# Kernel optimization log

Measured on AMD Instinct MI355X. Metric: run time of the kernel, lower is better.

The kernel has to match this reference:

```python
import jax, jax.numpy as jnp
import numpy as np
import math

NSAMPLE = 16
ATTN_TEMP = 1.0
LEAKY = 0.1
BN_EPS = 1e-5


def _knn(k, query, ref):
    # query [B,Nq,3], ref [B,Nr,3] -> idx [B,Nq,k] (indices into ref, nearest first)
    d = (jnp.sum(query * query, -1)[:, :, None]
         + jnp.sum(ref * ref, -1)[:, None, :]
         - 2.0 * jnp.einsum('bqc,brc->bqr', query, ref))
    _, idx = jax.lax.top_k(-d, k)
    return idx


def _gather(pts, idx):
    # pts [B,N,C], idx [B,M,K] -> [B,M,K,C]
    return jax.vmap(lambda p, i: p[i])(pts, idx)


def _bn_eval(x, g, b):
    # eval-mode BatchNorm2d with running_mean=0, running_var=1
    return x * (g / jnp.sqrt(1.0 + BN_EPS)) + b


def _leaky(x):
    return jnp.where(x >= 0, x, LEAKY * x)


def setup_inputs() -> dict:
    key = jax.random.key(0)
    ks = jax.random.split(key, 25)
    B, N, D, Cm, H = 2, 4096, 64, 64, 8
    f = jax.random.normal
    inp = {
        'xyz1': f(ks[0], (B, 3, N), jnp.float32),
        'xyz2': f(ks[1], (B, 3, N), jnp.float32),
        'xyz2w': f(ks[2], (B, 3, N), jnp.float32),
        'points1': f(ks[3], (B, D, N), jnp.float32),
        'points2': f(ks[4], (B, D, N), jnp.float32),
        'mlp_W0': f(ks[5], (Cm, 2 * D + 3), jnp.float32) * 0.1,
        'mlp_b0': f(ks[6], (Cm,), jnp.float32) * 0.05,
        'mlp_W1': f(ks[7], (Cm, Cm), jnp.float32) * 0.1,
        'mlp_b1': f(ks[8], (Cm,), jnp.float32) * 0.05,
        'wn_W0': f(ks[9], (H, 3), jnp.float32) * 0.3,
        'wn_b0': f(ks[10], (H,), jnp.float32) * 0.05,
        'wn_g0': jax.random.uniform(ks[11], (H,), jnp.float32, 0.5, 1.5),
        'wn_be0': f(ks[12], (H,), jnp.float32) * 0.05,
        'wn_W1': f(ks[13], (H, H), jnp.float32) * 0.3,
        'wn_b1': f(ks[14], (H,), jnp.float32) * 0.05,
        'wn_g1': jax.random.uniform(ks[15], (H,), jnp.float32, 0.5, 1.5),
        'wn_be1': f(ks[16], (H,), jnp.float32) * 0.05,
        'wn_W2': f(ks[17], (Cm, H), jnp.float32) * 0.3,
        'wn_b2': f(ks[18], (Cm,), jnp.float32) * 0.05,
        'wn_g2': jax.random.uniform(ks[19], (Cm,), jnp.float32, 0.5, 1.5),
        'wn_be2': f(ks[20], (Cm,), jnp.float32) * 0.05,
    }
    return inp


def reference(xyz1, xyz2, xyz2w, points1, points2,
              mlp_W0, mlp_b0, mlp_W1, mlp_b1,
              wn_W0, wn_b0, wn_g0, wn_be0,
              wn_W1, wn_b1, wn_g1, wn_be1,
              wn_W2, wn_b2, wn_g2, wn_be2):
    K = NSAMPLE
    B, C, N1 = xyz1.shape  # C == 3
    p1 = xyz1.transpose(0, 2, 1)    # [B,N1,3]
    p2 = xyz2.transpose(0, 2, 1)
    p2w = xyz2w.transpose(0, 2, 1)
    f1 = points1.transpose(0, 2, 1)  # [B,N1,D]
    f2 = points2.transpose(0, 2, 1)

    def mlp(f):
        f = _leaky(jnp.einsum('bnkc,oc->bnko', f, mlp_W0) + mlp_b0)
        f = _leaky(jnp.einsum('bnkc,oc->bnko', f, mlp_W1) + mlp_b1)
        return f

    idx = _knn(K, p1, p2)
    dir_xyz = _gather(p2, idx) - p1[:, :, None, :]          # [B,N1,K,3]
    idxw = _knn(K, p1, p2w)
    dir_xyzw = _gather(p2w, idxw) - p1[:, :, None, :]

    g1 = jnp.broadcast_to(f1[:, :, None, :], (B, N1, K, f1.shape[-1]))
    feat = mlp(jnp.concatenate([g1, _gather(f2, idx), dir_xyz], -1))    # [B,N1,K,Cm]
    featw = mlp(jnp.concatenate([g1, _gather(f2, idxw), dir_xyzw], -1))  # [B,N1,K,Cm]

    # per-channel K x K attention, contracted over all N1 points
    wqk = jnp.einsum('bnkc,bnlc->bckl', feat, featw)        # [B,Cm,K,K]
    wqk = jnp.clip(jax.nn.softmax(wqk / ATTN_TEMP, -1) / math.sqrt(C), 1e-10)
    # sum over trailing K is pushed into the attention matrix (same math)
    costw = jnp.einsum('bnlc,bcl->bcn', featw, wqk.sum(-1))  # [B,Cm,N1]
    cost = jnp.einsum('bnlc,bcl->bcn', feat, wqk.sum(-2))    # [B,Cm,N1]

    # self-neighborhood aggregation with WeightNet (bn=True, eval mode)
    idx_s = _knn(K, p1, p1)
    dir_s = _gather(p1, idx_s) - p1[:, :, None, :]           # [B,N1,K,3]
    h = jax.nn.relu(_bn_eval(jnp.einsum('bnkc,oc->bnko', dir_s, wn_W0) + wn_b0, wn_g0, wn_be0))
    h = jax.nn.relu(_bn_eval(jnp.einsum('bnkc,oc->bnko', h, wn_W1) + wn_b1, wn_g1, wn_be1))
    w = jax.nn.relu(_bn_eval(jnp.einsum('bnkc,oc->bnko', h, wn_W2) + wn_b2, wn_g2, wn_be2))  # [B,N1,K,Cm]

    grouped = _gather(cost.transpose(0, 2, 1), idx_s) + _gather(costw.transpose(0, 2, 1), idx_s)  # [B,N1,K,Cm]
    return jnp.einsum('bnkc,bnkc->bcn', w, grouped)          # [B,Cm,N1]
```

## Files before the change

### kernel.cpp

```cpp
#include <hip/hip_runtime.h>
#include <math.h>

#define B_  2
#define N_  4096
#define K_  16
#define D_  64
#define CM_ 64
#define H_  8

#define NSEG  8
#define SEGSZ (N_ / NSEG)
#define QPB   256
#define LIM   16
#define BATCH 8
#define TAUS  512

__device__ __forceinline__ void ce64(unsigned long long& a, unsigned long long& b) {
    bool sw = b < a;
    unsigned long long lo = sw ? b : a;
    unsigned long long hi = sw ? a : b;
    a = lo; b = hi;
}
__device__ __forceinline__ void cef(float& a, float& b) {
    float lo = fminf(a, b), hi = fmaxf(a, b);
    a = lo; b = hi;
}

#define SORT16_(e, CE) do { \
    CE(e[0],e[1]); CE(e[2],e[3]); CE(e[4],e[5]); CE(e[6],e[7]); \
    CE(e[8],e[9]); CE(e[10],e[11]); CE(e[12],e[13]); CE(e[14],e[15]); \
    CE(e[0],e[2]); CE(e[1],e[3]); CE(e[4],e[6]); CE(e[5],e[7]); \
    CE(e[8],e[10]); CE(e[9],e[11]); CE(e[12],e[14]); CE(e[13],e[15]); \
    CE(e[1],e[2]); CE(e[5],e[6]); CE(e[9],e[10]); CE(e[13],e[14]); \
    CE(e[0],e[4]); CE(e[1],e[5]); CE(e[2],e[6]); CE(e[3],e[7]); \
    CE(e[8],e[12]); CE(e[9],e[13]); CE(e[10],e[14]); CE(e[11],e[15]); \
    CE(e[2],e[4]); CE(e[3],e[5]); CE(e[10],e[12]); CE(e[11],e[13]); \
    CE(e[1],e[2]); CE(e[3],e[4]); CE(e[5],e[6]); \
    CE(e[9],e[10]); CE(e[11],e[12]); CE(e[13],e[14]); \
    CE(e[0],e[8]); CE(e[1],e[9]); CE(e[2],e[10]); CE(e[3],e[11]); \
    CE(e[4],e[12]); CE(e[5],e[13]); CE(e[6],e[14]); CE(e[7],e[15]); \
    CE(e[4],e[8]); CE(e[5],e[9]); CE(e[6],e[10]); CE(e[7],e[11]); \
    CE(e[2],e[4]); CE(e[3],e[5]); CE(e[6],e[8]); CE(e[7],e[9]); \
    CE(e[10],e[12]); CE(e[11],e[13]); \
    CE(e[1],e[2]); CE(e[3],e[4]); CE(e[5],e[6]); CE(e[7],e[8]); \
    CE(e[9],e[10]); CE(e[11],e[12]); CE(e[13],e[14]); \
} while (0)

#define BMERGE16_(d, CE) do { \
    CE(d[0],d[8]); CE(d[1],d[9]); CE(d[2],d[10]); CE(d[3],d[11]); \
    CE(d[4],d[12]); CE(d[5],d[13]); CE(d[6],d[14]); CE(d[7],d[15]); \
    CE(d[0],d[4]); CE(d[1],d[5]); CE(d[2],d[6]); CE(d[3],d[7]); \
    CE(d[8],d[12]); CE(d[9],d[13]); CE(d[10],d[14]); CE(d[11],d[15]); \
    CE(d[0],d[2]); CE(d[1],d[3]); CE(d[4],d[6]); CE(d[5],d[7]); \
    CE(d[8],d[10]); CE(d[9],d[11]); CE(d[12],d[14]); CE(d[13],d[15]); \
    CE(d[0],d[1]); CE(d[2],d[3]); CE(d[4],d[5]); CE(d[6],d[7]); \
    CE(d[8],d[9]); CE(d[10],d[11]); CE(d[12],d[13]); CE(d[14],d[15]); \
} while (0)

__global__ __launch_bounds__(256) void knn_tau_kernel(
    const float* __restrict__ xyz1, const float* __restrict__ xyz2,
    const float* __restrict__ xyz2w,
    float* __restrict__ tauBuf)
{
    const int b = blockIdx.y, which = blockIdx.z;
    const float* q = xyz1 + (size_t)b * 3 * N_;
    const float* r = (which == 0 ? xyz2 : (which == 1 ? xyz2w : xyz1)) + (size_t)b * 3 * N_;

    const int tid = threadIdx.x;
    const int qi = blockIdx.x * QPB + tid;
    const float qx = q[qi], qy = q[N_ + qi], qz = q[2 * N_ + qi];
    const float qq = qx * qx + qy * qy + qz * qz;

    __shared__ float4 tile[TAUS];
    __shared__ float  bufS[LIM * QPB];

    float bd[K_];
#pragma unroll
    for (int i = 0; i < K_; ++i) bd[i] = 3.4e38f;
    float tau = 3.4e38f;
    float c = 0.5f * (qq - tau);
    c -= fabsf(c) * 0.0009765625f + 1e-20f;
    int cnt = 0;

    for (int j = tid; j < TAUS; j += QPB) {
        float x = r[j], y = r[N_ + j], z = r[2 * N_ + j];
        tile[j] = make_float4(x, y, z, -0.5f * (x * x + y * y + z * z));
    }
    __syncthreads();

    auto compactF = [&](int m_end) {
        float e[16];
#pragma unroll
        for (int m = 0; m < 16; ++m) {
            float sv = bufS[m * QPB + tid];
            float dv = fmaxf(qq - 2.0f * sv, 0.0f);
            e[m] = (m < m_end) ? dv : 3.4e38f;
        }
        SORT16_(e, cef);
#pragma unroll
        for (int i = 0; i < 16; ++i) bd[i] = fminf(bd[i], e[15 - i]);
        BMERGE16_(bd, cef);
        tau = fminf(tau, bd[K_ - 1]);
        c = 0.5f * (qq - tau);
        c -= fabsf(c) * 0.0009765625f + 1e-20f;
    };

    for (int j0 = 0; j0 < TAUS; j0 += BATCH) {
        float s8[BATCH];
#pragma unroll
        for (int u = 0; u < BATCH; ++u) {
            float4 t = tile[j0 + u];
            s8[u] = qx * t.x + (qy * t.y + (qz * t.z + t.w));
        }
#pragma unroll
        for (int u = 0; u < BATCH; ++u) {
            bufS[cnt * QPB + tid] = s8[u];
            cnt += (s8[u] > c) ? 1 : 0;
        }
        if (__any(cnt > 8)) { compactF(cnt); cnt = 0; }
    }
    if (__any(cnt != 0)) compactF(cnt);

    tauBuf[((size_t)b * 3 + which) * N_ + qi] = bd[K_ - 1];
}

__global__ __launch_bounds__(256) void knn_seg_kernel(
    const float* __restrict__ xyz1, const float* __restrict__ xyz2,
    const float* __restrict__ xyz2w,
    const float* __restrict__ tauBuf,
    float* __restrict__ segD, int* __restrict__ segI)
{
    const int b = blockIdx.y;
    const int which = blockIdx.z >> 3;
    const int seg   = blockIdx.z & 7;
    const float* q = xyz1 + (size_t)b * 3 * N_;
    const float* r = (which == 0 ? xyz2 : (which == 1 ? xyz2w : xyz1)) + (size_t)b * 3 * N_;

    const int tid = threadIdx.x;
    const int qi = blockIdx.x * QPB + tid;
    const float qx = q[qi], qy = q[N_ + qi], qz = q[2 * N_ + qi];
    const float qq = qx * qx + qy * qy + qz * qz;

    __shared__ float4 tile[SEGSZ];
    __shared__ int    bufI[LIM * QPB];

    unsigned long long bd[K_];
#pragma unroll
    for (int i = 0; i < K_; ++i) bd[i] = ~0ull;
    float tau = tauBuf[((size_t)b * 3 + which) * N_ + qi];
    float c = 0.5f * (qq - tau);
    c -= fabsf(c) * 0.0009765625f + 1e-20f;
    int cnt = 0;

    const int base0 = seg * SEGSZ;
    for (int j = tid; j < SEGSZ; j += QPB) {
        float x = r[base0 + j], y = r[N_ + base0 + j], z = r[2 * N_ + base0 + j];
        tile[j] = make_float4(x, y, z, -0.5f * (x * x + y * y + z * z));
    }
    __syncthreads();

    auto compact = [&](int m_end) {
        unsigned long long e[16];
#pragma unroll
        for (int m = 0; m < 16; ++m) {
            int j = bufI[m * QPB + tid] & (SEGSZ - 1);
            float4 t = tile[j];
            float dot = qx * t.x + qy * t.y + qz * t.z;
            float rr = -2.0f * t.w;
            float dv = fmaxf((qq + rr) - 2.0f * dot, 0.0f);
            unsigned long long key =
                ((unsigned long long)__float_as_uint(dv) << 32)
                | (unsigned)(base0 + j);
            e[m] = (m < m_end) ? key : ~0ull;
        }
        SORT16_(e, ce64);
#pragma unroll
        for (int i = 0; i < 16; ++i) {
            unsigned long long cand = e[15 - i];
            if (cand < bd[i]) bd[i] = cand;
        }
        BMERGE16_(bd, ce64);
        tau = fminf(tau, __uint_as_float((unsigned)(bd[K_ - 1] >> 32)));
        c = 0.5f * (qq - tau);
        c -= fabsf(c) * 0.0009765625f + 1e-20f;
    };

    for (int j0 = 0; j0 < SEGSZ; j0 += BATCH) {
        float s8[BATCH];
#pragma unroll
        for (int u = 0; u < BATCH; ++u) {
            float4 t = tile[j0 + u];
            s8[u] = qx * t.x + (qy * t.y + (qz * t.z + t.w));
        }
#pragma unroll
        for (int u = 0; u < BATCH; ++u) {
            bufI[cnt * QPB + tid] = j0 + u;
            cnt += (s8[u] > c) ? 1 : 0;
        }
        if (__any(cnt > 8)) { compact(cnt); cnt = 0; }
    }
    if (__any(cnt != 0)) compact(cnt);

    const size_t ob = (((size_t)(b * 3 + which) * NSEG + seg) * K_) * N_ + qi;
#pragma unroll
    for (int i = 0; i < K_; ++i) {
        segD[ob + (size_t)i * N_] = __uint_as_float((unsigned)(bd[i] >> 32));
        segI[ob + (size_t)i * N_] = (int)(unsigned)bd[i];
    }
}

__global__ __launch_bounds__(256) void knn_merge_kernel(
    const float* __restrict__ segD, const int* __restrict__ segI,
    int* __restrict__ idxA, int* __restrict__ idxB, int* __restrict__ idxS)
{
    const int b = blockIdx.y, which = blockIdx.z;
    const int qi = blockIdx.x * 256 + threadIdx.x;
    unsigned long long m[K_];
#pragma unroll
    for (int i = 0; i < K_; ++i) m[i] = ~0ull;
    for (int s = 0; s < NSEG; ++s) {
        const size_t ob = (((size_t)(b * 3 + which) * NSEG + s) * K_) * N_ + qi;
        for (int e = 0; e < K_; ++e) {
            unsigned long long key =
                ((unsigned long long)__float_as_uint(segD[ob + (size_t)e * N_]) << 32)
                | (unsigned)segI[ob + (size_t)e * N_];
            if (key >= m[K_ - 1]) break;
            m[K_ - 1] = key;
#pragma unroll
            for (int i = K_ - 1; i > 0; --i) {
                if (m[i] < m[i - 1]) {
                    unsigned long long t = m[i]; m[i] = m[i - 1]; m[i - 1] = t;
                }
            }
        }
    }
    int* outp = (which == 0 ? idxA : (which == 1 ? idxB : idxS));
    int* op = outp + ((size_t)b * N_ + qi) * K_;
#pragma unroll
    for (int i = 0; i < K_; ++i) op[i] = (int)(unsigned)m[i];
}

__global__ __launch_bounds__(256) void pre_gemm_kernel(
    const float* __restrict__ points1, const float* __restrict__ points2,
    const float* __restrict__ W0,
    float* __restrict__ G1, float* __restrict__ P2)
{
    const int b = blockIdx.y, which = blockIdx.z;
    const float* src = which ? points2 : points1;
    float* dst = which ? P2 : G1;
    const int woff = which ? 64 : 0;
    const int n0 = blockIdx.x * 64;
    const int tid = threadIdx.x;

    __shared__ float sW[64 * 65];
    __shared__ float sA[64 * 68];

    for (int i = tid; i < 4096; i += 256) {
        int c = i & 63, o = i >> 6;
        sW[c * 65 + o] = W0[o * 131 + woff + c];
    }
    for (int i = tid; i < 4096; i += 256) {
        int n = i & 63, c = i >> 6;
        sA[c * 68 + n] = src[((size_t)b * 64 + c) * N_ + n0 + n];
    }
    __syncthreads();

    const int o = tid & 63, qg = tid >> 6;
    float acc[16];
#pragma unroll
    for (int j = 0; j < 16; ++j) acc[j] = 0.f;
    for (int c = 0; c < 64; ++c) {
        float w = sW[c * 65 + o];
        const float4* ap = (const float4*)&sA[c * 68 + qg * 16];
#pragma unroll
        for (int m = 0; m < 4; ++m) {
            float4 a4 = ap[m];
            acc[4 * m + 0] += w * a4.x;
            acc[4 * m + 1] += w * a4.y;
            acc[4 * m + 2] += w * a4.z;
            acc[4 * m + 3] += w * a4.w;
        }
    }
#pragma unroll
    for (int j = 0; j < 16; ++j)
        dst[((size_t)b * N_ + n0 + qg * 16 + j) * 64 + o] = acc[j];
}

__global__ __launch_bounds__(256) void mlp2_kernel(
    const float* __restrict__ xyz1, const float* __restrict__ xyz2,
    const float* __restrict__ xyz2w,
    const int* __restrict__ idxA, const int* __restrict__ idxB,
    const float* __restrict__ G1, const float* __restrict__ P2,
    const float* __restrict__ W0, const float* __restrict__ b0,
    const float* __restrict__ W1, const float* __restrict__ b1,
    float* __restrict__ feat, float* __restrict__ featw)
{
    const int b = blockIdx.y, which = blockIdx.z;
    const int* idx = which ? idxB : idxA;
    const float* refxyz = (which ? xyz2w : xyz2) + (size_t)b * 3 * N_;
    float* outp = which ? featw : feat;
    const int n0 = blockIdx.x * 8;
    const int tid = threadIdx.x;
    const int w = tid >> 6, lane = tid & 63;

    __shared__ float sh0[64 * 132];
    __shared__ float sW1[64 * 68];
    __shared__ float sWc[3 * 64];
    __shared__ float sB0[64];
    __shared__ float sQ[3][8];
    __shared__ int   sIdx[128];

    for (int i = tid; i < 4096; i += 256) {
        int c = i & 63, o = i >> 6;
        sW1[c * 68 + o] = W1[o * 64 + c];
    }
    if (tid < 192) { int m = tid >> 6, o = tid & 63; sWc[m * 64 + o] = W0[o * 131 + 128 + m]; }
    if (tid < 64) sB0[tid] = b0[tid];
    if (tid < 24) { int m = tid >> 3, j = tid & 7; sQ[m][j] = xyz1[((size_t)b * 3 + m) * N_ + n0 + j]; }
    if (tid < 128) sIdx[tid] = idx[((size_t)b * N_ + n0 + (tid >> 4)) * K_ + (tid & 15)];
    __syncthreads();

    {
        const int o = lane;
        const float wc0 = sWc[o], wc1 = sWc[64 + o], wc2 = sWc[128 + o];
        const float bb0 = sB0[o];
#pragma unroll
        for (int p = 0; p < 2; ++p) {
            const int pl = w * 2 + p;
            const float g1 = G1[((size_t)b * N_ + n0 + pl) * 64 + o];
            const float qx = sQ[0][pl], qy = sQ[1][pl], qz = sQ[2][pl];
            for (int k = 0; k < K_; ++k) {
                const int row = pl * K_ + k;
                const int ii = sIdx[row];
                float p2 = P2[((size_t)b * N_ + ii) * 64 + o];
                float dx = refxyz[ii] - qx;
                float dy = refxyz[N_ + ii] - qy;
                float dz = refxyz[2 * N_ + ii] - qz;
                float h = g1 + p2 + dx * wc0 + dy * wc1 + dz * wc2 + bb0;
                h = h >= 0.f ? h : 0.1f * h;
                sh0[o * 132 + row] = h;
            }
        }
    }
    __syncthreads();

    const int lr = lane >> 3, lo = lane & 7;
    float accv[4][8];
    {
        float4 bva = *(const float4*)&b1[lo * 8];
        float4 bvb = *(const float4*)&b1[lo * 8 + 4];
#pragma unroll
        for (int dr = 0; dr < 4; ++dr) {
            accv[dr][0] = bva.x; accv[dr][1] = bva.y; accv[dr][2] = bva.z; accv[dr][3] = bva.w;
            accv[dr][4] = bvb.x; accv[dr][5] = bvb.y; accv[dr][6] = bvb.z; accv[dr][7] = bvb.w;
        }
    }
    for (int c = 0; c < 64; ++c) {
        float4 a4 = *(const float4*)&sh0[c * 132 + w * 32 + lr * 4];
        float4 wa = *(const float4*)&sW1[c * 68 + lo * 8];
        float4 wb = *(const float4*)&sW1[c * 68 + lo * 8 + 4];
        float av[4] = {a4.x, a4.y, a4.z, a4.w};
        float wv[8] = {wa.x, wa.y, wa.z, wa.w, wb.x, wb.y, wb.z, wb.w};
#pragma unroll
        for (int dr = 0; dr < 4; ++dr)
#pragma unroll
            for (int j = 0; j < 8; ++j)
                accv[dr][j] += av[dr] * wv[j];
    }
#pragma unroll
    for (int dr = 0; dr < 4; ++dr) {
        const int row = w * 32 + lr * 4 + dr;
        const int pl = row >> 4, k = row & 15;
        float o8[8];
#pragma unroll
        for (int j = 0; j < 8; ++j) {
            float v = accv[dr][j];
            o8[j] = v >= 0.f ? v : 0.1f * v;
        }
        float* op = outp + (((size_t)b * N_ + n0 + pl) * K_ + k) * 64 + lo * 8;
        *(float4*)op = make_float4(o8[0], o8[1], o8[2], o8[3]);
        *(float4*)(op + 4) = make_float4(o8[4], o8[5], o8[6], o8[7]);
    }
}

#define NCHUNK 32
#define CG 16
#define NITER ((N_ / NCHUNK) / 16)

__global__ __launch_bounds__(256) void attn_partial_kernel(
    const float* __restrict__ feat, const float* __restrict__ featw,
    float* __restrict__ partial)
{
    const int chunk = blockIdx.x;
    const int b = blockIdx.y >> 2;
    const int c0 = (blockIdx.y & 3) * CG;
    const int tid = threadIdx.x;
    const int k = tid >> 4, c = tid & 15;

    __shared__ float sf[16 * 16 * 17];
    __shared__ float sfw[16 * 16 * 20];

    float acc[K_];
#pragma unroll
    for (int l = 0; l < K_; ++l) acc[l] = 0.f;

    const int n0 = chunk * (N_ / NCHUNK);
    float rf[16], rfw[16];

    auto LOADG = [&](int ns) {
#pragma unroll
        for (int t = 0; t < 16; ++t) {
            int i = tid + t * 256;
            int nn = i >> 8, p = (i >> 4) & 15, qv = i & 15;
            size_t base = (((size_t)b * N_ + n0 + ns + nn) * K_ + p) * CM_ + c0 + qv;
            rf[t]  = feat[base];
            rfw[t] = featw[base];
        }
    };
    auto STORE = [&]() {
#pragma unroll
        for (int t = 0; t < 16; ++t) {
            int i = tid + t * 256;
            int nn = i >> 8, p = (i >> 4) & 15, qv = i & 15;
            sf[nn * 272 + p * 17 + qv]  = rf[t];
            sfw[nn * 320 + qv * 20 + p] = rfw[t];
        }
    };

    LOADG(0);
    for (int it = 0; it < NITER; ++it) {
        __syncthreads();
        STORE();
        __syncthreads();
        if (it + 1 < NITER) LOADG((it + 1) * 16);
#pragma unroll
        for (int nn = 0; nn < 16; ++nn) {
            float f = sf[nn * 272 + k * 17 + c];
            const float4* fp = (const float4*)&sfw[nn * 320 + c * 20];
#pragma unroll
            for (int m = 0; m < 4; ++m) {
                float4 v = fp[m];
                acc[4 * m + 0] += f * v.x;
                acc[4 * m + 1] += f * v.y;
                acc[4 * m + 2] += f * v.z;
                acc[4 * m + 3] += f * v.w;
            }
        }
    }
    float* pp = partial + ((((size_t)b * NCHUNK + chunk) * CM_ + (c0 + c)) * K_ + k) * K_;
#pragma unroll
    for (int m = 0; m < 4; ++m)
        *(float4*)(pp + 4 * m) = make_float4(acc[4 * m], acc[4 * m + 1], acc[4 * m + 2], acc[4 * m + 3]);
}

__global__ __launch_bounds__(256) void attn_reduce_kernel(
    const float* __restrict__ partial,
    float* __restrict__ rowsum, float* __restrict__ colsum)
{
    const int c = blockIdx.x, b = blockIdx.y;
    const int tid = threadIdx.x;
    const int k = tid >> 4, l = tid & 15;
    __shared__ float smat[K_][K_ + 1];

    float acc = 0.f;
#pragma unroll
    for (int ch = 0; ch < NCHUNK; ++ch)
        acc += partial[((((size_t)b * NCHUNK + ch) * CM_ + c) * K_ + k) * K_ + l];

    float m = acc;
#pragma unroll
    for (int off = 8; off >= 1; off >>= 1) m = fmaxf(m, __shfl_xor(m, off, 16));
    float e = expf(acc - m);
    float s = e;
#pragma unroll
    for (int off = 8; off >= 1; off >>= 1) s += __shfl_xor(s, off, 16);
    float sm = fmaxf((e / s) * 0.57735026918962576f, 1e-10f);

    float rs = sm;
#pragma unroll
    for (int off = 8; off >= 1; off >>= 1) rs += __shfl_xor(rs, off, 16);
    if (l == 0) rowsum[((size_t)b * CM_ + c) * K_ + k] = rs;

    smat[k][l] = sm;
    __syncthreads();
    if (tid < K_) {
        float cs = 0.f;
#pragma unroll
        for (int kk = 0; kk < K_; ++kk) cs += smat[kk][tid];
        colsum[((size_t)b * CM_ + c) * K_ + tid] = cs;
    }
}

__global__ __launch_bounds__(256) void cost_kernel(
    const float* __restrict__ feat, const float* __restrict__ featw,
    const float* __restrict__ rowsum, const float* __restrict__ colsum,
    float* __restrict__ costT, float* __restrict__ costwT)
{
    const int b = blockIdx.y;
    const int tid = threadIdx.x;
    __shared__ float scs[64][K_ + 1], srs[64][K_ + 1];
    for (int i = tid; i < 64 * K_; i += 256) {
        int cc = i >> 4, j = i & 15;
        scs[cc][j] = colsum[((size_t)b * CM_ + cc) * K_ + j];
        srs[cc][j] = rowsum[((size_t)b * CM_ + cc) * K_ + j];
    }
    __syncthreads();
    const int ng = tid >> 6, c = tid & 63;
    const int n = blockIdx.x * 4 + ng;
    const float* fp  = feat  + (((size_t)b * N_ + n) * K_) * 64 + c;
    const float* fwp = featw + (((size_t)b * N_ + n) * K_) * 64 + c;
    float a = 0.f, aw = 0.f;
#pragma unroll
    for (int j = 0; j < K_; ++j) {
        a  += fp[j * 64]  * scs[c][j];
        aw += fwp[j * 64] * srs[c][j];
    }
    costT[((size_t)b * N_ + n) * 64 + c]  = a;
    costwT[((size_t)b * N_ + n) * 64 + c] = aw;
}

__global__ __launch_bounds__(256) void final_kernel(
    const float* __restrict__ xyz1,
    const int* __restrict__ idxS,
    const float* __restrict__ costT, const float* __restrict__ costwT,
    const float* __restrict__ wn_W0, const float* __restrict__ wn_b0,
    const float* __restrict__ wn_g0, const float* __restrict__ wn_be0,
    const float* __restrict__ wn_W1, const float* __restrict__ wn_b1,
    const float* __restrict__ wn_g1, const float* __restrict__ wn_be1,
    const float* __restrict__ wn_W2, const float* __restrict__ wn_b2,
    const float* __restrict__ wn_g2, const float* __restrict__ wn_be2,
    float* __restrict__ out)
{
    const int b = blockIdx.y;
    const int tid = threadIdx.x;
    const int ng = tid >> 6, c = tid & 63;
    const int n = blockIdx.x * 4 + ng;
    const float invs = 1.0f / sqrtf(1.0f + 1e-5f);

    __shared__ int   sI[4][K_];
    __shared__ float sH1[4][K_][H_];

    if (c < K_) {
        const int k = c;
        const float* qb = xyz1 + (size_t)b * 3 * N_;
        int ii = idxS[((size_t)b * N_ + n) * K_ + k];
        sI[ng][k] = ii;
        float dx = qb[ii] - qb[n];
        float dy = qb[N_ + ii] - qb[N_ + n];
        float dz = qb[2 * N_ + ii] - qb[2 * N_ + n];
        float h0[H_];
#pragma unroll
        for (int o = 0; o < H_; ++o) {
            float v = wn_W0[o * 3] * dx + wn_W0[o * 3 + 1] * dy + wn_W0[o * 3 + 2] * dz + wn_b0[o];
            v = v * (wn_g0[o] * invs) + wn_be0[o];
            h0[o] = fmaxf(v, 0.f);
        }
#pragma unroll
        for (int o = 0; o < H_; ++o) {
            float v = wn_b1[o];
#pragma unroll
            for (int j = 0; j < H_; ++j) v += wn_W1[o * H_ + j] * h0[j];
            v = v * (wn_g1[o] * invs) + wn_be1[o];
            sH1[ng][k][o] = fmaxf(v, 0.f);
        }
    }
    __syncthreads();

    float w2r[H_];
#pragma unroll
    for (int j = 0; j < H_; ++j) w2r[j] = wn_W2[c * H_ + j];
    const float b2v = wn_b2[c];
    const float s2v = wn_g2[c] * invs;
    const float t2v = wn_be2[c];

    float acc = 0.f;
#pragma unroll
    for (int k = 0; k < K_; ++k) {
        float v = b2v;
#pragma unroll
        for (int j = 0; j < H_; ++j) v += w2r[j] * sH1[ng][k][j];
        float wv = fmaxf(v * s2v + t2v, 0.f);
        int ii = sI[ng][k];
        size_t base = ((size_t)b * N_ + ii) * 64 + c;
        acc += wv * (costT[base] + costwT[base]);
    }
    out[((size_t)b * CM_ + c) * N_ + n] = acc;
}

extern "C" void kernel_launch(void* const* d_in, const int* in_sizes, int n_in,
                              void* d_out, int out_size, void* d_ws, size_t ws_size,
                              hipStream_t stream)
{
    const float* xyz1    = (const float*)d_in[0];
    const float* xyz2    = (const float*)d_in[1];
    const float* xyz2w   = (const float*)d_in[2];
    const float* points1 = (const float*)d_in[3];
    const float* points2 = (const float*)d_in[4];
    const float* mlp_W0  = (const float*)d_in[5];
    const float* mlp_b0  = (const float*)d_in[6];
    const float* mlp_W1  = (const float*)d_in[7];
    const float* mlp_b1  = (const float*)d_in[8];
    const float* wn_W0   = (const float*)d_in[9];
    const float* wn_b0   = (const float*)d_in[10];
    const float* wn_g0   = (const float*)d_in[11];
    const float* wn_be0  = (const float*)d_in[12];
    const float* wn_W1   = (const float*)d_in[13];
    const float* wn_b1   = (const float*)d_in[14];
    const float* wn_g1   = (const float*)d_in[15];
    const float* wn_be1  = (const float*)d_in[16];
    const float* wn_W2   = (const float*)d_in[17];
    const float* wn_b2   = (const float*)d_in[18];
    const float* wn_g2   = (const float*)d_in[19];
    const float* wn_be2  = (const float*)d_in[20];
    float* out = (float*)d_out;

    char* ws = (char*)d_ws;
    size_t off = 0;
    auto alloc = [&](size_t bytes) -> void* {
        void* p = ws + off;
        off += (bytes + 255) & ~(size_t)255;
        return p;
    };
    int*   idxA   = (int*)  alloc((size_t)B_ * N_ * K_ * sizeof(int));
    int*   idxB   = (int*)  alloc((size_t)B_ * N_ * K_ * sizeof(int));
    int*   idxS   = (int*)  alloc((size_t)B_ * N_ * K_ * sizeof(int));
    float* tauBuf = (float*)alloc((size_t)B_ * 3 * N_ * sizeof(float));
    float* feat   = (float*)alloc((size_t)B_ * N_ * K_ * CM_ * sizeof(float));
    float* featw  = (float*)alloc((size_t)B_ * N_ * K_ * CM_ * sizeof(float));
    float* rowsum = (float*)alloc((size_t)B_ * CM_ * K_ * sizeof(float));
    float* colsum = (float*)alloc((size_t)B_ * CM_ * K_ * sizeof(float));
    float* costT  = (float*)alloc((size_t)B_ * N_ * CM_ * sizeof(float));
    float* costwT = (float*)alloc((size_t)B_ * N_ * CM_ * sizeof(float));
    (void)ws_size; (void)in_sizes; (void)n_in; (void)out_size;

    float* segD    = feat;
    int*   segI    = (int*)featw;
    float* G1      = costT;
    float* P2      = costwT;
    float* partial = costT;

    pre_gemm_kernel<<<dim3(N_ / 64, B_, 2), 256, 0, stream>>>(points1, points2, mlp_W0, G1, P2);
    knn_tau_kernel<<<dim3(N_ / QPB, B_, 3), QPB, 0, stream>>>(
        xyz1, xyz2, xyz2w, tauBuf);
    knn_seg_kernel<<<dim3(N_ / QPB, B_, 3 * NSEG), QPB, 0, stream>>>(
        xyz1, xyz2, xyz2w, tauBuf, segD, segI);
    knn_merge_kernel<<<dim3(N_ / 256, B_, 3), 256, 0, stream>>>(
        segD, segI, idxA, idxB, idxS);
    mlp2_kernel<<<dim3(N_ / 8, B_, 2), 256, 0, stream>>>(
        xyz1, xyz2, xyz2w, idxA, idxB, G1, P2,
        mlp_W0, mlp_b0, mlp_W1, mlp_b1, feat, featw);
    attn_partial_kernel<<<dim3(NCHUNK, 4 * B_), 256, 0, stream>>>(feat, featw, partial);
    attn_reduce_kernel<<<dim3(CM_, B_), 256, 0, stream>>>(partial, rowsum, colsum);
    cost_kernel<<<dim3(N_ / 4, B_), 256, 0, stream>>>(feat, featw, rowsum, colsum, costT, costwT);
    final_kernel<<<dim3(N_ / 4, B_), 256, 0, stream>>>(xyz1, idxS, costT, costwT,
                                                       wn_W0, wn_b0, wn_g0, wn_be0,
                                                       wn_W1, wn_b1, wn_g1, wn_be1,
                                                       wn_W2, wn_b2, wn_g2, wn_be2, out);
}
```

Before: 238.5 us.

## Pre-pack reference points as float4 and stream KNN tiles from global memory

Adds a pack kernel that writes each reference cloud once as float4 (x, y, z, -0.5*|r|^2). The KNN tau and segment kernels then read these packed points through uniform global loads with register double-buffering, replacing the per-block shared-memory tile build and its barrier. This removes the repeated tile construction and cuts shared-memory use, at the cost of an extra launch and global or cache traffic. Compaction now does a random-index global load instead of an LDS read. A k-loop in the MLP kernel is also marked for unrolling.

New measurement: 249.4 us. 4.6% more time.

```diff
diff --git a/kernel.cpp b/kernel.cpp
--- a/kernel.cpp
+++ b/kernel.cpp
@@ -57,22 +57,33 @@
     CE(d[8],d[9]); CE(d[10],d[11]); CE(d[12],d[13]); CE(d[14],d[15]); \
 } while (0)
 
+__global__ __launch_bounds__(256) void pack_kernel(
+    const float* __restrict__ xyz1, const float* __restrict__ xyz2,
+    const float* __restrict__ xyz2w, float4* __restrict__ packed)
+{
+    const int b = blockIdx.y, which = blockIdx.z;
+    const float* r = (which == 0 ? xyz2 : (which == 1 ? xyz2w : xyz1)) + (size_t)b * 3 * N_;
+    const int j = blockIdx.x * 256 + threadIdx.x;
+    float x = r[j], y = r[N_ + j], z = r[2 * N_ + j];
+    packed[((size_t)which * B_ + b) * N_ + j] =
+        make_float4(x, y, z, -0.5f * (x * x + y * y + z * z));
+}
+
 __global__ __launch_bounds__(256) void knn_tau_kernel(
-    const float* __restrict__ xyz1, const float* __restrict__ xyz2,
-    const float* __restrict__ xyz2w,
+    const float* __restrict__ xyz1,
+    const float4* __restrict__ packed,
     float* __restrict__ tauBuf)
 {
     const int b = blockIdx.y, which = blockIdx.z;
     const float* q = xyz1 + (size_t)b * 3 * N_;
-    const float* r = (which == 0 ? xyz2 : (which == 1 ? xyz2w : xyz1)) + (size_t)b * 3 * N_;
+    const float4* __restrict__ pk = packed + ((size_t)which * B_ + b) * N_;
 
     const int tid = threadIdx.x;
     const int qi = blockIdx.x * QPB + tid;
     const float qx = q[qi], qy = q[N_ + qi], qz = q[2 * N_ + qi];
     const float qq = qx * qx + qy * qy + qz * qz;
 
-    __shared__ float4 tile[TAUS];
-    __shared__ float  bufS[LIM * QPB];
+    __shared__ float bufS[LIM * QPB];
 
     float bd[K_];
 #pragma unroll
@@ -81,12 +92,6 @@
     float c = 0.5f * (qq - tau);
     c -= fabsf(c) * 0.0009765625f + 1e-20f;
     int cnt = 0;
-
-    for (int j = tid; j < TAUS; j += QPB) {
-        float x = r[j], y = r[N_ + j], z = r[2 * N_ + j];
-        tile[j] = make_float4(x, y, z, -0.5f * (x * x + y * y + z * z));
-    }
-    __syncthreads();
 
     auto compactF = [&](int m_end) {
         float e[16];
@@ -105,11 +110,18 @@
         c -= fabsf(c) * 0.0009765625f + 1e-20f;
     };
 
+    float4 cur[BATCH], nxt[BATCH];
+#pragma unroll
+    for (int u = 0; u < BATCH; ++u) cur[u] = pk[u];
     for (int j0 = 0; j0 < TAUS; j0 += BATCH) {
+        if (j0 + BATCH < TAUS) {
+#pragma unroll
+            for (int u = 0; u < BATCH; ++u) nxt[u] = pk[j0 + BATCH + u];
+        }
         float s8[BATCH];
 #pragma unroll
         for (int u = 0; u < BATCH; ++u) {
-            float4 t = tile[j0 + u];
+            float4 t = cur[u];
             s8[u] = qx * t.x + (qy * t.y + (qz * t.z + t.w));
         }
 #pragma unroll
@@ -118,6 +130,8 @@
             cnt += (s8[u] > c) ? 1 : 0;
         }
         if (__any(cnt > 8)) { compactF(cnt); cnt = 0; }
+#pragma unroll
+        for (int u = 0; u < BATCH; ++u) cur[u] = nxt[u];
     }
     if (__any(cnt != 0)) compactF(cnt);
 
@@ -125,8 +139,8 @@
 }
 
 __global__ __launch_bounds__(256) void knn_seg_kernel(
-    const float* __restrict__ xyz1, const float* __restrict__ xyz2,
-    const float* __restrict__ xyz2w,
+    const float* __restrict__ xyz1,
+    const float4* __restrict__ packed,
     const float* __restrict__ tauBuf,
     float* __restrict__ segD, int* __restrict__ segI)
 {
@@ -134,15 +148,15 @@
     const int which = blockIdx.z >> 3;
     const int seg   = blockIdx.z & 7;
     const float* q = xyz1 + (size_t)b * 3 * N_;
-    const float* r = (which == 0 ? xyz2 : (which == 1 ? xyz2w : xyz1)) + (size_t)b * 3 * N_;
+    const int base0 = seg * SEGSZ;
+    const float4* __restrict__ pk = packed + ((size_t)which * B_ + b) * N_ + base0;
 
     const int tid = threadIdx.x;
     const int qi = blockIdx.x * QPB + tid;
     const float qx = q[qi], qy = q[N_ + qi], qz = q[2 * N_ + qi];
     const float qq = qx * qx + qy * qy + qz * qz;
 
-    __shared__ float4 tile[SEGSZ];
-    __shared__ int    bufI[LIM * QPB];
+    __shared__ int bufI[LIM * QPB];
 
     unsigned long long bd[K_];
 #pragma unroll
@@ -152,19 +166,12 @@
     c -= fabsf(c) * 0.0009765625f + 1e-20f;
     int cnt = 0;
 
-    const int base0 = seg * SEGSZ;
-    for (int j = tid; j < SEGSZ; j += QPB) {
-        float x = r[base0 + j], y = r[N_ + base0 + j], z = r[2 * N_ + base0 + j];
-        tile[j] = make_float4(x, y, z, -0.5f * (x * x + y * y + z * z));
-    }
-    __syncthreads();
-
     auto compact = [&](int m_end) {
         unsigned long long e[16];
 #pragma unroll
         for (int m = 0; m < 16; ++m) {
             int j = bufI[m * QPB + tid] & (SEGSZ - 1);
-            float4 t = tile[j];
+            float4 t = pk[j];
             float dot = qx * t.x + qy * t.y + qz * t.z;
             float rr = -2.0f * t.w;
             float dv = fmaxf((qq + rr) - 2.0f * dot, 0.0f);
@@ -185,11 +192,18 @@
         c -= fabsf(c) * 0.0009765625f + 1e-20f;
     };
 
+    float4 cur[BATCH], nxt[BATCH];
+#pragma unroll
+    for (int u = 0; u < BATCH; ++u) cur[u] = pk[u];
     for (int j0 = 0; j0 < SEGSZ; j0 += BATCH) {
+        if (j0 + BATCH < SEGSZ) {
+#pragma unroll
+            for (int u = 0; u < BATCH; ++u) nxt[u] = pk[j0 + BATCH + u];
+        }
         float s8[BATCH];
 #pragma unroll
         for (int u = 0; u < BATCH; ++u) {
-            float4 t = tile[j0 + u];
+            float4 t = cur[u];
             s8[u] = qx * t.x + (qy * t.y + (qz * t.z + t.w));
         }
 #pragma unroll
@@ -198,6 +212,8 @@
             cnt += (s8[u] > c) ? 1 : 0;
         }
         if (__any(cnt > 8)) { compact(cnt); cnt = 0; }
+#pragma unroll
+        for (int u = 0; u < BATCH; ++u) cur[u] = nxt[u];
     }
     if (__any(cnt != 0)) compact(cnt);
 
@@ -329,6 +345,7 @@
             const int pl = w * 2 + p;
             const float g1 = G1[((size_t)b * N_ + n0 + pl) * 64 + o];
             const float qx = sQ[0][pl], qy = sQ[1][pl], qz = sQ[2][pl];
+#pragma unroll
             for (int k = 0; k < K_; ++k) {
                 const int row = pl * K_ + k;
                 const int ii = sIdx[row];
@@ -621,16 +638,17 @@
         off += (bytes + 255) & ~(size_t)255;
         return p;
     };
-    int*   idxA   = (int*)  alloc((size_t)B_ * N_ * K_ * sizeof(int));
-    int*   idxB   = (int*)  alloc((size_t)B_ * N_ * K_ * sizeof(int));
-    int*   idxS   = (int*)  alloc((size_t)B_ * N_ * K_ * sizeof(int));
-    float* tauBuf = (float*)alloc((size_t)B_ * 3 * N_ * sizeof(float));
-    float* feat   = (float*)alloc((size_t)B_ * N_ * K_ * CM_ * sizeof(float));
-    float* featw  = (float*)alloc((size_t)B_ * N_ * K_ * CM_ * sizeof(float));
-    float* rowsum = (float*)alloc((size_t)B_ * CM_ * K_ * sizeof(float));
-    float* colsum = (float*)alloc((size_t)B_ * CM_ * K_ * sizeof(float));
-    float* costT  = (float*)alloc((size_t)B_ * N_ * CM_ * sizeof(float));
-    float* costwT = (float*)alloc((size_t)B_ * N_ * CM_ * sizeof(float));
+    int*    idxA   = (int*)   alloc((size_t)B_ * N_ * K_ * sizeof(int));
+    int*    idxB   = (int*)   alloc((size_t)B_ * N_ * K_ * sizeof(int));
+    int*    idxS   = (int*)   alloc((size_t)B_ * N_ * K_ * sizeof(int));
+    float*  tauBuf = (float*) alloc((size_t)B_ * 3 * N_ * sizeof(float));
+    float4* packed = (float4*)alloc((size_t)3 * B_ * N_ * sizeof(float4));
+    float*  feat   = (float*) alloc((size_t)B_ * N_ * K_ * CM_ * sizeof(float));
+    float*  featw  = (float*) alloc((size_t)B_ * N_ * K_ * CM_ * sizeof(float));
+    float*  rowsum = (float*) alloc((size_t)B_ * CM_ * K_ * sizeof(float));
+    float*  colsum = (float*) alloc((size_t)B_ * CM_ * K_ * sizeof(float));
+    float*  costT  = (float*) alloc((size_t)B_ * N_ * CM_ * sizeof(float));
+    float*  costwT = (float*) alloc((size_t)B_ * N_ * CM_ * sizeof(float));
     (void)ws_size; (void)in_sizes; (void)n_in; (void)out_size;
 
     float* segD    = feat;
@@ -639,11 +657,12 @@
     float* P2      = costwT;
     float* partial = costT;
 
+    pack_kernel<<<dim3(N_ / 256, B_, 3), 256, 0, stream>>>(xyz1, xyz2, xyz2w, packed);
     pre_gemm_kernel<<<dim3(N_ / 64, B_, 2), 256, 0, stream>>>(points1, points2, mlp_W0, G1, P2);
     knn_tau_kernel<<<dim3(N_ / QPB, B_, 3), QPB, 0, stream>>>(
-        xyz1, xyz2, xyz2w, tauBuf);
+        xyz1, packed, tauBuf);
     knn_seg_kernel<<<dim3(N_ / QPB, B_, 3 * NSEG), QPB, 0, stream>>>(
-        xyz1, xyz2, xyz2w, tauBuf, segD, segI);
+        xyz1, packed, tauBuf, segD, segI);
     knn_merge_kernel<<<dim3(N_ / 256, B_, 3), 256, 0, stream>>>(
         segD, segI, idxA, idxB, idxS);
     mlp2_kernel<<<dim3(N_ / 8, B_, 2), 256, 0, stream>>>(
```
